# Kernel optimization log

Hardware: AMD Instinct MI355X
Metric: run time of the kernel (lower is better)

The kernel has to match this reference:

```python
import jax, jax.numpy as jnp
import numpy as np

NEG_INF = -1e9

def setup_inputs() -> dict:
    key = jax.random.key(0)
    k1, k2, k3, k4, k5 = jax.random.split(key, 5)
    N, F_IN, F_OUT, H = 8192, 128, 32, 4
    node_features = jax.random.normal(k1, (N, F_IN), dtype=jnp.float32)
    adj_matrix = jax.random.randint(k2, (N, N), 0, 2, dtype=jnp.int32)
    # stacked per-head params (original: one Linear W [F_IN,F_OUT] + attention vec a [2*F_OUT] per head)
    W = jax.random.normal(k3, (H, F_IN, F_OUT), dtype=jnp.float32) * (1.0 / np.sqrt(F_IN))
    a_src = jax.random.normal(k4, (H, F_OUT), dtype=jnp.float32) * 0.1
    a_dst = jax.random.normal(k5, (H, F_OUT), dtype=jnp.float32) * 0.1
    return {"node_features": node_features, "adj_matrix": adj_matrix,
            "W": W, "a_src": a_src, "a_dst": a_dst}

def reference(node_features, adj_matrix, W, a_src, a_dst):
    alpha = 0.2  # LeakyReLU negative slope
    # project: [H, N, F_OUT]
    h = jnp.einsum('nf,hfo->hno', node_features, W)
    # GAT scores e_ij = LeakyReLU(a_src . h_i + a_dst . h_j), shape [H, N, N]
    e_src = jnp.einsum('hno,ho->hn', h, a_src)  # [H, N]
    e_dst = jnp.einsum('hno,ho->hn', h, a_dst)  # [H, N]
    e = jax.nn.leaky_relu(e_src[:, :, None] + e_dst[:, None, :], negative_slope=alpha)
    mask = (adj_matrix > 0)[None, :, :]
    attn = jax.nn.softmax(jnp.where(mask, e, NEG_INF), axis=-1)  # [H, N, N]
    out = jnp.einsum('hij,hjo->hio', attn, h)  # [H, N, F_OUT]
    # concat heads along feature dim -> [N, H*F_OUT]
    H_, N_, O_ = out.shape
    return jnp.transpose(out, (1, 0, 2)).reshape(N_, H_ * O_)
```

## Files before the change

### kernel.cpp

```cpp
#include <hip/hip_runtime.h>
#include <hip/hip_bf16.h>

#define NTOT 8192
#define FIN 128
#define FOUT 32
#define NH 4
#define NSEG 4
#define LOG2E 1.4426950408889634f
#define BUFB 18432

typedef __attribute__((ext_vector_type(4))) float f32x4;
typedef __attribute__((ext_vector_type(4))) unsigned int u32x4;
typedef __attribute__((ext_vector_type(8))) __bf16 bf16x8;
typedef unsigned long long u64;
typedef unsigned int u32;

__device__ __forceinline__ unsigned short f2bf(float x) {
  __hip_bfloat16 h = __float2bfloat16(x);
  return *reinterpret_cast<unsigned short*>(&h);
}

__device__ __forceinline__ float fexp2(float y) {
  float p;
  asm("v_exp_f32 %0, %1" : "=v"(p) : "v"(y));
  return p;
}

__global__ __launch_bounds__(512, 2) void k0_pack(
    const int* __restrict__ adj, u64* __restrict__ bits64T) {
  int row = blockIdx.x * 8 + (threadIdx.x >> 6);
  int l = threadIdx.x & 63;
  const int* ap = adj + (size_t)row * NTOT + l;
  u64* bp = bits64T + row;
#pragma unroll 4
  for (int j64 = 0; j64 < NTOT / 64; ++j64) {
    int v = ap[j64 * 64];
    u64 mske = __ballot(v != 0);
    if (l == 0) bp[(size_t)j64 * NTOT] = mske;
  }
}

__global__ __launch_bounds__(256, 2) void k1_project(
    const float* __restrict__ X, const float* __restrict__ W,
    float* __restrict__ h, unsigned short* __restrict__ panel) {
  __shared__ float Xs[32 * 128];
  __shared__ float Ws[32 * 128];
  __shared__ unsigned short Hs[128 * 40];
  int t = threadIdx.x;
  int nb = blockIdx.x * 32;

  const f32x4* Xg = reinterpret_cast<const f32x4*>(X + (size_t)nb * FIN);
  f32x4* Xs4 = reinterpret_cast<f32x4*>(Xs);
#pragma unroll
  for (int r = 0; r < 4; ++r) Xs4[t + r * 256] = Xg[t + r * 256];

  int ng = t >> 5, oq = t & 31;
  int n0 = ng * 4, o0 = oq * 4;
  f32x4 acc[4];
#pragma unroll
  for (int nn = 0; nn < 4; ++nn) acc[nn] = (f32x4){0.f, 0.f, 0.f, 0.f};

  for (int kp = 0; kp < 4; ++kp) {
    __syncthreads();
#pragma unroll
    for (int r = 0; r < 4; ++r) {
      int q = t + r * 256;
      int flat = q * 4;
      int kk = flat >> 7;
      int c = flat & 127;
      int hdd = c >> 5;
      int oo = c & 31;
      *reinterpret_cast<f32x4*>(&Ws[kk * 128 + c]) =
          *reinterpret_cast<const f32x4*>(W + hdd * (FIN * FOUT) +
                                          (kp * 32 + kk) * FOUT + oo);
    }
    __syncthreads();
#pragma unroll 8
    for (int kk = 0; kk < 32; ++kk) {
      f32x4 wv = *reinterpret_cast<const f32x4*>(&Ws[kk * 128 + o0]);
#pragma unroll
      for (int nn = 0; nn < 4; ++nn)
        acc[nn] += Xs[(n0 + nn) * 128 + kp * 32 + kk] * wv;
    }
  }
#pragma unroll
  for (int nn = 0; nn < 4; ++nn) {
    *reinterpret_cast<f32x4*>(&h[(size_t)(nb + n0 + nn) * 128 + o0]) = acc[nn];
#pragma unroll
    for (int c = 0; c < 4; ++c)
      Hs[(o0 + c) * 40 + (n0 + nn)] = f2bf(acc[nn][c]);
  }
  __syncthreads();
  int jt = blockIdx.x;
#pragma unroll
  for (int it = 0; it < 2; ++it) {
    int item = t + it * 256;
    int p = item >> 6;
    int l = item & 63;
    int o = p * 16 + (l & 15);
    u32x4 v = *reinterpret_cast<const u32x4*>(&Hs[o * 40 + (l >> 4) * 8]);
    *reinterpret_cast<u32x4*>(panel + (size_t)(p * 256 + jt) * 512 + l * 8) = v;
  }
}

__global__ __launch_bounds__(256, 2) void k2_scores(
    const float* __restrict__ h, const float* __restrict__ a_src,
    const float* __restrict__ a_dst, float* __restrict__ Sl2,
    float* __restrict__ Dt) {
  int n = blockIdx.x * 256 + threadIdx.x;
  const f32x4* hv = reinterpret_cast<const f32x4*>(h + (size_t)n * 128);
  const f32x4* as4 = reinterpret_cast<const f32x4*>(a_src);
  const f32x4* ad4 = reinterpret_cast<const f32x4*>(a_dst);
#pragma unroll
  for (int hd = 0; hd < NH; ++hd) {
    f32x4 sa = {0.f, 0.f, 0.f, 0.f}, da = {0.f, 0.f, 0.f, 0.f};
#pragma unroll
    for (int q = 0; q < 8; ++q) {
      f32x4 x = hv[hd * 8 + q];
      sa += x * as4[hd * 8 + q];
      da += x * ad4[hd * 8 + q];
    }
    float s = (sa[0] + sa[1]) + (sa[2] + sa[3]);
    float d = (da[0] + da[1]) + (da[2] + da[3]);
    Sl2[hd * NTOT + n] = s * LOG2E;
    Dt[(n >> 6) * 256 + hd * 64 + (n & 63)] = d * LOG2E;
  }
}

__global__ __launch_bounds__(512)
__attribute__((amdgpu_waves_per_eu(4, 4))) void k3_attn(
    const u64* __restrict__ bits64T, const float* __restrict__ Sl2,
    const float* __restrict__ Dt, const unsigned short* __restrict__ panel,
    float* __restrict__ pacc, float* __restrict__ plsum) {
  const int N = NTOT;
  __shared__ char smem[2 * BUFB];
  int tid = threadIdx.x;
  int w = tid >> 6, l = tid & 63;
  int hd = w & 3, isub = w >> 2;
  int itile = blockIdx.x >> 2, seg = blockIdx.x & 3;
  int ibase = itile * 64 + isub * 32;
  int iblk = itile * 64;
  int m = l & 15, jc = (l >> 4) * 8;
  int i0 = ibase + m, i1 = i0 + 16;
  float sv0 = Sl2[hd * N + i0], sv1 = Sl2[hd * N + i1];
  int seg0 = seg * 32;

  const char* psrc =
      (const char*)panel + ((size_t)w * 256) * 1024 + (size_t)l * 16;
  const char* dsrc = (const char*)Dt + (size_t)l * 16;
  const u64* bsrc = bits64T + iblk + l;

  f32x4 z4 = {0.f, 0.f, 0.f, 0.f};
  f32x4 acc0[2] = {z4, z4}, acc1[2] = {z4, z4}, acc2[2] = {z4, z4};
  bf16x8 bones;
  {
    u32 pat = (m == 0) ? 0x3f803f80u : 0u;
    u32x4 tmp = {pat, pat, pat, pat};
    bones = *reinterpret_cast<bf16x8*>(&tmp);
  }

  u32x4 Pr0, Pr1, Dr;
  u64 Br;

#define LOADR(t_)                                              \
  {                                                            \
    int tc_ = (t_) > 31 ? 31 : (t_);                           \
    size_t jm_ = (size_t)(seg0 + tc_);                         \
    Pr0 = *(const u32x4*)(psrc + jm_ * 2048);                  \
    Pr1 = *(const u32x4*)(psrc + jm_ * 2048 + 1024);           \
    if (w == 0) Br = bsrc[jm_ * N];                            \
    if (w == 1) Dr = *(const u32x4*)(dsrc + jm_ * 1024);       \
  }

#define DSW(cb_)                                               \
  {                                                            \
    char* b_ = smem + (cb_)*BUFB;                              \
    *(u32x4*)(b_ + w * 2048 + l * 16) = Pr0;                   \
    *(u32x4*)(b_ + w * 2048 + 1024 + l * 16) = Pr1;            \
    if (w == 0) *(u64*)(b_ + 17408 + l * 8) = Br;              \
    if (w == 1) *(u32x4*)(b_ + 16384 + l * 16) = Dr;           \
  }

#define K3_AF(AF, BY, DA, DB, SV)                                        \
  {                                                                      \
    f32x4 xa_ = (DA) + (SV);                                             \
    f32x4 xb_ = (DB) + (SV);                                             \
    f32x4 ya_ = __builtin_elementwise_max(xa_, 0.2f * xa_);              \
    f32x4 yb_ = __builtin_elementwise_max(xb_, 0.2f * xb_);              \
    bf16x8 af_;                                                          \
    _Pragma("unroll") for (int e = 0; e < 4; ++e) af_[e] =               \
        (__bf16)fexp2(ya_[e]);                                           \
    _Pragma("unroll") for (int e = 0; e < 4; ++e) af_[e + 4] =           \
        (__bf16)fexp2(yb_[e]);                                           \
    u32x4 mk_;                                                           \
    _Pragma("unroll") for (int p = 0; p < 4; ++p) {                      \
      u32 lo_ = (u32)(((int)((BY) << (31 - 2 * p))) >> 31);              \
      u32 hi_ = (u32)(((int)((BY) << (30 - 2 * p))) >> 31);              \
      mk_[p] = __builtin_amdgcn_perm(hi_, lo_, 0x07060100u);             \
    }                                                                    \
    u32x4 av_ = *reinterpret_cast<u32x4*>(&af_) & mk_;                   \
    AF = *reinterpret_cast<bf16x8*>(&av_);                               \
  }

#define K3_RG(AF, B0, B1, RG)                                                \
  acc0[RG] =                                                                 \
      __builtin_amdgcn_mfma_f32_16x16x32_bf16(AF, (B0), acc0[RG], 0, 0, 0);  \
  acc1[RG] =                                                                 \
      __builtin_amdgcn_mfma_f32_16x16x32_bf16(AF, (B1), acc1[RG], 0, 0, 0);  \
  acc2[RG] =                                                                 \
      __builtin_amdgcn_mfma_f32_16x16x32_bf16(AF, bones, acc2[RG], 0, 0, 0);

#define COMPUTE(cb_)                                                     \
  {                                                                      \
    const char* b_ = smem + (cb_)*BUFB;                                  \
    u64 w0 = *(const u64*)(b_ + 17408 + (isub * 32 + m) * 8);            \
    u64 w1 = *(const u64*)(b_ + 17408 + (isub * 32 + 16 + m) * 8);       \
    const char* dp_ = b_ + 16384 + hd * 256 + jc * 4;                    \
    f32x4 d0 = *(const f32x4*)(dp_);                                     \
    f32x4 d1 = *(const f32x4*)(dp_ + 16);                                \
    f32x4 d2 = *(const f32x4*)(dp_ + 128);                               \
    f32x4 d3 = *(const f32x4*)(dp_ + 144);                               \
    const char* pp_ = b_ + (hd * 2) * 2048 + l * 16;                     \
    bf16x8 B0a = *(const bf16x8*)(pp_);                                  \
    bf16x8 B0b = *(const bf16x8*)(pp_ + 1024);                           \
    bf16x8 B1a = *(const bf16x8*)(pp_ + 2048);                           \
    bf16x8 B1b = *(const bf16x8*)(pp_ + 3072);                           \
    bf16x8 af_r;                                                         \
    u32 by_;                                                             \
    by_ = ((u32)w0 >> jc) & 0xFFu;                                       \
    K3_AF(af_r, by_, d0, d1, sv0) K3_RG(af_r, B0a, B1a, 0)               \
    by_ = ((u32)w1 >> jc) & 0xFFu;                                       \
    K3_AF(af_r, by_, d0, d1, sv1) K3_RG(af_r, B0a, B1a, 1)               \
    by_ = ((u32)(w0 >> 32) >> jc) & 0xFFu;                               \
    K3_AF(af_r, by_, d2, d3, sv0) K3_RG(af_r, B0b, B1b, 0)               \
    by_ = ((u32)(w1 >> 32) >> jc) & 0xFFu;                               \
    K3_AF(af_r, by_, d2, d3, sv1) K3_RG(af_r, B0b, B1b, 1)               \
  }

  LOADR(0);
  DSW(0);
  LOADR(1);
  __syncthreads();

#pragma unroll 1
  for (int t = 0; t < 32; ++t) {
    int cur = t & 1;
    COMPUTE(cur);
    DSW(cur ^ 1);
    LOADR(t + 2);
    __syncthreads();
  }
#undef LOADR
#undef DSW
#undef K3_AF
#undef K3_RG
#undef COMPUTE

#pragma unroll
  for (int rg = 0; rg < 2; ++rg) {
    int rb = ibase + rg * 16 + ((l >> 4) << 2);
    if (m == 0) {
#pragma unroll
      for (int r = 0; r < 4; ++r)
        plsum[(seg * NH + hd) * N + rb + r] = acc2[rg][r];
    }
#pragma unroll
    for (int r = 0; r < 4; ++r) {
      int row = rb + r;
      pacc[((size_t)seg * N + row) * 128 + hd * 32 + m] = acc0[rg][r];
      pacc[((size_t)seg * N + row) * 128 + hd * 32 + 16 + m] = acc1[rg][r];
    }
  }
}

__global__ __launch_bounds__(256, 2) void k4_combine(
    const float* __restrict__ pacc, const float* __restrict__ plsum,
    float* __restrict__ out) {
  int idx = blockIdx.x * 256 + threadIdx.x;
  int i = idx >> 7;
  int c = idx & 127;
  int hd = c >> 5;
  float a = 0.f, ls = 0.f;
#pragma unroll
  for (int s = 0; s < NSEG; ++s) {
    a += pacc[((size_t)s * NTOT + i) * 128 + c];
    ls += plsum[(s * NH + hd) * NTOT + i];
  }
  out[idx] = (ls > 0.f) ? a / ls : 0.f;
}

extern "C" void kernel_launch(void* const* d_in, const int* in_sizes, int n_in,
                              void* d_out, int out_size, void* d_ws,
                              size_t ws_size, hipStream_t stream) {
  const float* X = (const float*)d_in[0];
  const int* adj = (const int*)d_in[1];
  const float* W = (const float*)d_in[2];
  const float* a_src = (const float*)d_in[3];
  const float* a_dst = (const float*)d_in[4];
  float* out = (float*)d_out;

  char* ws = (char*)d_ws;
  float* h = (float*)(ws + 0x0);
  unsigned short* panel = (unsigned short*)(ws + 0x400000);
  float* Sl2 = (float*)(ws + 0x600000);
  float* Dt = (float*)(ws + 0x620000);
  u64* bits64T = (u64*)(ws + 0x640000);
  float* pacc = (float*)(ws + 0xE40000);
  float* plsum = (float*)(ws + 0x1E40000);

  k0_pack<<<dim3(1024), dim3(512), 0, stream>>>(adj, bits64T);
  k1_project<<<dim3(256), dim3(256), 0, stream>>>(X, W, h, panel);
  k2_scores<<<dim3(32), dim3(256), 0, stream>>>(h, a_src, a_dst, Sl2, Dt);
  k3_attn<<<dim3(128 * NSEG), dim3(512), 0, stream>>>(bits64T, Sl2, Dt, panel,
                                                      pacc, plsum);
  k4_combine<<<dim3(4096), dim3(256), 0, stream>>>(pacc, plsum, out);
}
```

Before: 178.3 us.

## Restructure attention kernel to per-wave async LDS DMA with no block barriers

The attention kernel now runs 4 waves per block, one per head, and each wave covers all 64 rows instead of 32, so the B operands from LDS are reused across four row groups. Tile data (panel, Dt, adjacency bits) goes straight from global memory into each wave's private double-buffered LDS region through global_load_lds DMA. Manual vmcnt waits replace __syncthreads, so no register staging or block-wide barrier is needed. In exchange, each wave holds more accumulators and issues redundant Dt and bitmask loads per head. Occupancy is pinned to 2 waves per EU, and correctness depends on the hand-counted vmcnt values.

```diff
diff --git a/kernel.cpp b/kernel.cpp
--- a/kernel.cpp
+++ b/kernel.cpp
@@ -7,7 +7,7 @@
 #define NH 4
 #define NSEG 4
 #define LOG2E 1.4426950408889634f
-#define BUFB 18432
+#define WBUF 4864
 
 typedef __attribute__((ext_vector_type(4))) float f32x4;
 typedef __attribute__((ext_vector_type(4))) unsigned int u32x4;
@@ -24,6 +24,17 @@
   float p;
   asm("v_exp_f32 %0, %1" : "=v"(p) : "v"(y));
   return p;
+}
+
+__device__ __forceinline__ void dma16(const void* g, void* l) {
+  __builtin_amdgcn_global_load_lds(
+      (const __attribute__((address_space(1))) void*)g,
+      (__attribute__((address_space(3))) void*)l, 16, 0, 0);
+}
+__device__ __forceinline__ void dma4(const void* g, void* l) {
+  __builtin_amdgcn_global_load_lds(
+      (const __attribute__((address_space(1))) void*)g,
+      (__attribute__((address_space(3))) void*)l, 4, 0, 0);
 }
 
 __global__ __launch_bounds__(512, 2) void k0_pack(
@@ -127,31 +138,35 @@
   }
 }
 
-__global__ __launch_bounds__(512)
-__attribute__((amdgpu_waves_per_eu(4, 4))) void k3_attn(
+__global__ __launch_bounds__(256)
+__attribute__((amdgpu_waves_per_eu(2, 2))) void k3_attn(
     const u64* __restrict__ bits64T, const float* __restrict__ Sl2,
     const float* __restrict__ Dt, const unsigned short* __restrict__ panel,
     float* __restrict__ pacc, float* __restrict__ plsum) {
   const int N = NTOT;
-  __shared__ char smem[2 * BUFB];
+  __shared__ char smem[4 * 2 * WBUF];
   int tid = threadIdx.x;
-  int w = tid >> 6, l = tid & 63;
-  int hd = w & 3, isub = w >> 2;
+  int hd = tid >> 6, l = tid & 63;
   int itile = blockIdx.x >> 2, seg = blockIdx.x & 3;
-  int ibase = itile * 64 + isub * 32;
-  int iblk = itile * 64;
+  int ibase = itile * 64;
   int m = l & 15, jc = (l >> 4) * 8;
-  int i0 = ibase + m, i1 = i0 + 16;
-  float sv0 = Sl2[hd * N + i0], sv1 = Sl2[hd * N + i1];
+  char* wbase = smem + hd * (2 * WBUF);
+
+  float sv0 = Sl2[hd * N + ibase + m];
+  float sv1 = Sl2[hd * N + ibase + 16 + m];
+  float sv2 = Sl2[hd * N + ibase + 32 + m];
+  float sv3 = Sl2[hd * N + ibase + 48 + m];
+  asm volatile("" : "+v"(sv0), "+v"(sv1), "+v"(sv2), "+v"(sv3));
   int seg0 = seg * 32;
 
-  const char* psrc =
-      (const char*)panel + ((size_t)w * 256) * 1024 + (size_t)l * 16;
-  const char* dsrc = (const char*)Dt + (size_t)l * 16;
-  const u64* bsrc = bits64T + iblk + l;
+  const char* pg0 = (const char*)panel + (size_t)(hd * 2) * 262144;
+  const char* pg1 = pg0 + 262144;
+  const char* dg = (const char*)Dt;
+  const char* bg = (const char*)bits64T;
 
   f32x4 z4 = {0.f, 0.f, 0.f, 0.f};
-  f32x4 acc0[2] = {z4, z4}, acc1[2] = {z4, z4}, acc2[2] = {z4, z4};
+  f32x4 acc0[4] = {z4, z4, z4, z4}, acc1[4] = {z4, z4, z4, z4},
+        acc2[4] = {z4, z4, z4, z4};
   bf16x8 bones;
   {
     u32 pat = (m == 0) ? 0x3f803f80u : 0u;
@@ -159,26 +174,44 @@
     bones = *reinterpret_cast<bf16x8*>(&tmp);
   }
 
-  u32x4 Pr0, Pr1, Dr;
-  u64 Br;
-
-#define LOADR(t_)                                              \
-  {                                                            \
-    int tc_ = (t_) > 31 ? 31 : (t_);                           \
-    size_t jm_ = (size_t)(seg0 + tc_);                         \
-    Pr0 = *(const u32x4*)(psrc + jm_ * 2048);                  \
-    Pr1 = *(const u32x4*)(psrc + jm_ * 2048 + 1024);           \
-    if (w == 0) Br = bsrc[jm_ * N];                            \
-    if (w == 1) Dr = *(const u32x4*)(dsrc + jm_ * 1024);       \
-  }
-
-#define DSW(cb_)                                               \
-  {                                                            \
-    char* b_ = smem + (cb_)*BUFB;                              \
-    *(u32x4*)(b_ + w * 2048 + l * 16) = Pr0;                   \
-    *(u32x4*)(b_ + w * 2048 + 1024 + l * 16) = Pr1;            \
-    if (w == 0) *(u64*)(b_ + 17408 + l * 8) = Br;              \
-    if (w == 1) *(u32x4*)(b_ + 16384 + l * 16) = Dr;           \
+#define STAGE(t_)                                                      \
+  {                                                                    \
+    int tc_ = (t_) > 31 ? 31 : (t_);                                   \
+    size_t jm_ = (size_t)(seg0 + tc_);                                 \
+    char* lb_ = wbase + ((t_)&1) * WBUF;                               \
+    const char* g0_ = pg0 + jm_ * 2048 + (size_t)l * 16;               \
+    const char* g1_ = pg1 + jm_ * 2048 + (size_t)l * 16;               \
+    dma16(g0_, lb_);                                                   \
+    dma16(g0_ + 1024, lb_ + 1024);                                     \
+    dma16(g1_, lb_ + 2048);                                            \
+    dma16(g1_ + 1024, lb_ + 3072);                                     \
+    dma4(dg + jm_ * 1024 + hd * 256 + (size_t)l * 4, lb_ + 4096);      \
+    const char* gb_ = bg + (jm_ * N + ibase) * 8;                      \
+    dma4(gb_ + (size_t)l * 4, lb_ + 4352);                             \
+    dma4(gb_ + 256 + (size_t)l * 4, lb_ + 4608);                       \
+  }
+
+  u64 wr0, wr1, wr2, wr3;
+  f32x4 d0, d1, d2, d3;
+  bf16x8 B0a, B0b, B1a, B1b;
+
+#define LDSREAD(cb_)                                                   \
+  {                                                                    \
+    const char* b_ = wbase + (cb_)*WBUF;                               \
+    wr0 = *(const u64*)(b_ + 4352 + m * 8);                            \
+    wr1 = *(const u64*)(b_ + 4352 + 128 + m * 8);                      \
+    wr2 = *(const u64*)(b_ + 4352 + 256 + m * 8);                      \
+    wr3 = *(const u64*)(b_ + 4352 + 384 + m * 8);                      \
+    const char* dp_ = b_ + 4096 + jc * 4;                              \
+    d0 = *(const f32x4*)(dp_);                                         \
+    d1 = *(const f32x4*)(dp_ + 16);                                    \
+    d2 = *(const f32x4*)(dp_ + 128);                                   \
+    d3 = *(const f32x4*)(dp_ + 144);                                   \
+    const char* pp_ = b_ + (size_t)l * 16;                             \
+    B0a = *(const bf16x8*)(pp_);                                       \
+    B0b = *(const bf16x8*)(pp_ + 1024);                                \
+    B1a = *(const bf16x8*)(pp_ + 2048);                                \
+    B1b = *(const bf16x8*)(pp_ + 3072);                                \
   }
 
 #define K3_AF(AF, BY, DA, DB, SV)                                        \
@@ -202,62 +235,52 @@
     AF = *reinterpret_cast<bf16x8*>(&av_);                               \
   }
 
-#define K3_RG(AF, B0, B1, RG)                                                \
-  acc0[RG] =                                                                 \
-      __builtin_amdgcn_mfma_f32_16x16x32_bf16(AF, (B0), acc0[RG], 0, 0, 0);  \
-  acc1[RG] =                                                                 \
-      __builtin_amdgcn_mfma_f32_16x16x32_bf16(AF, (B1), acc1[RG], 0, 0, 0);  \
-  acc2[RG] =                                                                 \
-      __builtin_amdgcn_mfma_f32_16x16x32_bf16(AF, bones, acc2[RG], 0, 0, 0);
-
-#define COMPUTE(cb_)                                                     \
-  {                                                                      \
-    const char* b_ = smem + (cb_)*BUFB;                                  \
-    u64 w0 = *(const u64*)(b_ + 17408 + (isub * 32 + m) * 8);            \
-    u64 w1 = *(const u64*)(b_ + 17408 + (isub * 32 + 16 + m) * 8);       \
-    const char* dp_ = b_ + 16384 + hd * 256 + jc * 4;                    \
-    f32x4 d0 = *(const f32x4*)(dp_);                                     \
-    f32x4 d1 = *(const f32x4*)(dp_ + 16);                                \
-    f32x4 d2 = *(const f32x4*)(dp_ + 128);                               \
-    f32x4 d3 = *(const f32x4*)(dp_ + 144);                               \
-    const char* pp_ = b_ + (hd * 2) * 2048 + l * 16;                     \
-    bf16x8 B0a = *(const bf16x8*)(pp_);                                  \
-    bf16x8 B0b = *(const bf16x8*)(pp_ + 1024);                           \
-    bf16x8 B1a = *(const bf16x8*)(pp_ + 2048);                           \
-    bf16x8 B1b = *(const bf16x8*)(pp_ + 3072);                           \
-    bf16x8 af_r;                                                         \
-    u32 by_;                                                             \
-    by_ = ((u32)w0 >> jc) & 0xFFu;                                       \
-    K3_AF(af_r, by_, d0, d1, sv0) K3_RG(af_r, B0a, B1a, 0)               \
-    by_ = ((u32)w1 >> jc) & 0xFFu;                                       \
-    K3_AF(af_r, by_, d0, d1, sv1) K3_RG(af_r, B0a, B1a, 1)               \
-    by_ = ((u32)(w0 >> 32) >> jc) & 0xFFu;                               \
-    K3_AF(af_r, by_, d2, d3, sv0) K3_RG(af_r, B0b, B1b, 0)               \
-    by_ = ((u32)(w1 >> 32) >> jc) & 0xFFu;                               \
-    K3_AF(af_r, by_, d2, d3, sv1) K3_RG(af_r, B0b, B1b, 1)               \
-  }
-
-  LOADR(0);
-  DSW(0);
-  LOADR(1);
-  __syncthreads();
+#define MATH_RG(RG, WR, SV)                                                  \
+  {                                                                          \
+    bf16x8 af_r;                                                             \
+    u32 by_ = ((u32)(WR) >> jc) & 0xFFu;                                     \
+    K3_AF(af_r, by_, d0, d1, SV)                                             \
+    acc0[RG] =                                                               \
+        __builtin_amdgcn_mfma_f32_16x16x32_bf16(af_r, B0a, acc0[RG], 0, 0, 0); \
+    acc1[RG] =                                                               \
+        __builtin_amdgcn_mfma_f32_16x16x32_bf16(af_r, B1a, acc1[RG], 0, 0, 0); \
+    acc2[RG] = __builtin_amdgcn_mfma_f32_16x16x32_bf16(af_r, bones,          \
+                                                       acc2[RG], 0, 0, 0);   \
+    by_ = ((u32)((WR) >> 32) >> jc) & 0xFFu;                                 \
+    K3_AF(af_r, by_, d2, d3, SV)                                             \
+    acc0[RG] =                                                               \
+        __builtin_amdgcn_mfma_f32_16x16x32_bf16(af_r, B0b, acc0[RG], 0, 0, 0); \
+    acc1[RG] =                                                               \
+        __builtin_amdgcn_mfma_f32_16x16x32_bf16(af_r, B1b, acc1[RG], 0, 0, 0); \
+    acc2[RG] = __builtin_amdgcn_mfma_f32_16x16x32_bf16(af_r, bones,          \
+                                                       acc2[RG], 0, 0, 0);   \
+  }
+
+  STAGE(0)
+  STAGE(1)
 
 #pragma unroll 1
   for (int t = 0; t < 32; ++t) {
     int cur = t & 1;
-    COMPUTE(cur);
-    DSW(cur ^ 1);
-    LOADR(t + 2);
-    __syncthreads();
-  }
-#undef LOADR
-#undef DSW
+    asm volatile("s_waitcnt vmcnt(7)" ::: "memory");
+    LDSREAD(cur)
+    asm volatile("s_waitcnt lgkmcnt(0)" ::: "memory");
+    __builtin_amdgcn_sched_barrier(0);
+    STAGE(t + 2)
+    MATH_RG(0, wr0, sv0)
+    MATH_RG(1, wr1, sv1)
+    MATH_RG(2, wr2, sv2)
+    MATH_RG(3, wr3, sv3)
+  }
+#undef STAGE
+#undef LDSREAD
 #undef K3_AF
-#undef K3_RG
-#undef COMPUTE
-
-#pragma unroll
-  for (int rg = 0; rg < 2; ++rg) {
+#undef MATH_RG
+
+  asm volatile("s_waitcnt vmcnt(0)" ::: "memory");
+
+#pragma unroll
+  for (int rg = 0; rg < 4; ++rg) {
     int rb = ibase + rg * 16 + ((l >> 4) << 2);
     if (m == 0) {
 #pragma unroll
@@ -311,7 +334,7 @@
   k0_pack<<<dim3(1024), dim3(512), 0, stream>>>(adj, bits64T);
   k1_project<<<dim3(256), dim3(256), 0, stream>>>(X, W, h, panel);
   k2_scores<<<dim3(32), dim3(256), 0, stream>>>(h, a_src, a_dst, Sl2, Dt);
-  k3_attn<<<dim3(128 * NSEG), dim3(512), 0, stream>>>(bits64T, Sl2, Dt, panel,
+  k3_attn<<<dim3(128 * NSEG), dim3(256), 0, stream>>>(bits64T, Sl2, Dt, panel,
                                                       pacc, plsum);
   k4_combine<<<dim3(4096), dim3(256), 0, stream>>>(pacc, plsum, out);
 }
```

Result: no change. 178.2 us (-0.1%).

## Fuse adjacency bit-packing into attention kernel and drop LDS staging

Applied to the files above, without the earlier changes.

Removes the separate bit-packing kernel and has the attention kernel read the int32 adjacency rows directly, using a select to -1e9 before exp for masking. Each wave now owns 16 rows across all four heads, with the panel and Dt loaded straight from global memory instead of being staged through shared memory with barriers. Adjacency loads are double-buffered in registers. The aim is to avoid the extra pass that writes and re-reads the packed mask, plus the block synchronisation. The cost is that the attention kernel now streams the full 256MB int32 adjacency itself, and the panel and Dt are re-read per wave from cache.

```diff
diff --git a/kernel.cpp b/kernel.cpp
--- a/kernel.cpp
+++ b/kernel.cpp
@@ -6,10 +6,11 @@
 #define FOUT 32
 #define NH 4
 #define NSEG 4
+#define SEGJ (NTOT / NSEG)
 #define LOG2E 1.4426950408889634f
-#define BUFB 18432
 
 typedef __attribute__((ext_vector_type(4))) float f32x4;
+typedef __attribute__((ext_vector_type(4))) int i32x4;
 typedef __attribute__((ext_vector_type(4))) unsigned int u32x4;
 typedef __attribute__((ext_vector_type(8))) __bf16 bf16x8;
 typedef unsigned long long u64;
@@ -24,20 +25,6 @@
   float p;
   asm("v_exp_f32 %0, %1" : "=v"(p) : "v"(y));
   return p;
-}
-
-__global__ __launch_bounds__(512, 2) void k0_pack(
-    const int* __restrict__ adj, u64* __restrict__ bits64T) {
-  int row = blockIdx.x * 8 + (threadIdx.x >> 6);
-  int l = threadIdx.x & 63;
-  const int* ap = adj + (size_t)row * NTOT + l;
-  u64* bp = bits64T + row;
-#pragma unroll 4
-  for (int j64 = 0; j64 < NTOT / 64; ++j64) {
-    int v = ap[j64 * 64];
-    u64 mske = __ballot(v != 0);
-    if (l == 0) bp[(size_t)j64 * NTOT] = mske;
-  }
 }
 
 __global__ __launch_bounds__(256, 2) void k1_project(
@@ -127,31 +114,29 @@
   }
 }
 
-__global__ __launch_bounds__(512)
-__attribute__((amdgpu_waves_per_eu(4, 4))) void k3_attn(
-    const u64* __restrict__ bits64T, const float* __restrict__ Sl2,
+__global__ __launch_bounds__(256)
+__attribute__((amdgpu_waves_per_eu(2, 2))) void k3_attn(
+    const int* __restrict__ adj, const float* __restrict__ Sl2,
     const float* __restrict__ Dt, const unsigned short* __restrict__ panel,
     float* __restrict__ pacc, float* __restrict__ plsum) {
   const int N = NTOT;
-  __shared__ char smem[2 * BUFB];
   int tid = threadIdx.x;
   int w = tid >> 6, l = tid & 63;
-  int hd = w & 3, isub = w >> 2;
   int itile = blockIdx.x >> 2, seg = blockIdx.x & 3;
-  int ibase = itile * 64 + isub * 32;
-  int iblk = itile * 64;
-  int m = l & 15, jc = (l >> 4) * 8;
-  int i0 = ibase + m, i1 = i0 + 16;
-  float sv0 = Sl2[hd * N + i0], sv1 = Sl2[hd * N + i1];
+  int ibase = itile * 64;
+  int m = l & 15, g = l >> 4, jc = g * 8;
+  int row = ibase + w * 16 + m;
   int seg0 = seg * 32;
 
-  const char* psrc =
-      (const char*)panel + ((size_t)w * 256) * 1024 + (size_t)l * 16;
-  const char* dsrc = (const char*)Dt + (size_t)l * 16;
-  const u64* bsrc = bits64T + iblk + l;
+  float svv[4];
+#pragma unroll
+  for (int hd = 0; hd < 4; ++hd) svv[hd] = Sl2[hd * N + row];
+
+  const int* adjr = adj + (size_t)row * N + seg * SEGJ + jc;
 
   f32x4 z4 = {0.f, 0.f, 0.f, 0.f};
-  f32x4 acc0[2] = {z4, z4}, acc1[2] = {z4, z4}, acc2[2] = {z4, z4};
+  f32x4 c0[4] = {z4, z4, z4, z4}, c1[4] = {z4, z4, z4, z4},
+        cs[4] = {z4, z4, z4, z4};
   bf16x8 bones;
   {
     u32 pat = (m == 0) ? 0x3f803f80u : 0u;
@@ -159,116 +144,91 @@
     bones = *reinterpret_cast<bf16x8*>(&tmp);
   }
 
-  u32x4 Pr0, Pr1, Dr;
-  u64 Br;
-
-#define LOADR(t_)                                              \
+  i32x4 Aa0, Aa1, Aa2, Aa3, Ba0, Ba1, Ba2, Ba3;
+
+#define AISS(P, t_)                                            \
   {                                                            \
     int tc_ = (t_) > 31 ? 31 : (t_);                           \
-    size_t jm_ = (size_t)(seg0 + tc_);                         \
-    Pr0 = *(const u32x4*)(psrc + jm_ * 2048);                  \
-    Pr1 = *(const u32x4*)(psrc + jm_ * 2048 + 1024);           \
-    if (w == 0) Br = bsrc[jm_ * N];                            \
-    if (w == 1) Dr = *(const u32x4*)(dsrc + jm_ * 1024);       \
-  }
-
-#define DSW(cb_)                                               \
-  {                                                            \
-    char* b_ = smem + (cb_)*BUFB;                              \
-    *(u32x4*)(b_ + w * 2048 + l * 16) = Pr0;                   \
-    *(u32x4*)(b_ + w * 2048 + 1024 + l * 16) = Pr1;            \
-    if (w == 0) *(u64*)(b_ + 17408 + l * 8) = Br;              \
-    if (w == 1) *(u32x4*)(b_ + 16384 + l * 16) = Dr;           \
-  }
-
-#define K3_AF(AF, BY, DA, DB, SV)                                        \
+    const int* a_ = adjr + tc_ * 64;                           \
+    P##a0 = *reinterpret_cast<const i32x4*>(a_);               \
+    P##a1 = *reinterpret_cast<const i32x4*>(a_ + 4);           \
+    P##a2 = *reinterpret_cast<const i32x4*>(a_ + 32);          \
+    P##a3 = *reinterpret_cast<const i32x4*>(a_ + 36);          \
+  }                                                            \
+  __builtin_amdgcn_sched_barrier(0);
+
+#define AFSEL(AF, AV0, AV1, DA, DB, SV)                                  \
   {                                                                      \
     f32x4 xa_ = (DA) + (SV);                                             \
     f32x4 xb_ = (DB) + (SV);                                             \
     f32x4 ya_ = __builtin_elementwise_max(xa_, 0.2f * xa_);              \
     f32x4 yb_ = __builtin_elementwise_max(xb_, 0.2f * xb_);              \
-    bf16x8 af_;                                                          \
-    _Pragma("unroll") for (int e = 0; e < 4; ++e) af_[e] =               \
-        (__bf16)fexp2(ya_[e]);                                           \
-    _Pragma("unroll") for (int e = 0; e < 4; ++e) af_[e + 4] =           \
-        (__bf16)fexp2(yb_[e]);                                           \
-    u32x4 mk_;                                                           \
-    _Pragma("unroll") for (int p = 0; p < 4; ++p) {                      \
-      u32 lo_ = (u32)(((int)((BY) << (31 - 2 * p))) >> 31);              \
-      u32 hi_ = (u32)(((int)((BY) << (30 - 2 * p))) >> 31);              \
-      mk_[p] = __builtin_amdgcn_perm(hi_, lo_, 0x07060100u);             \
+    _Pragma("unroll") for (int e = 0; e < 4; ++e) {                      \
+      float y_ = ((AV0)[e] != 0) ? ya_[e] : -1e9f;                       \
+      AF[e] = (__bf16)fexp2(y_);                                         \
     }                                                                    \
-    u32x4 av_ = *reinterpret_cast<u32x4*>(&af_) & mk_;                   \
-    AF = *reinterpret_cast<bf16x8*>(&av_);                               \
-  }
-
-#define K3_RG(AF, B0, B1, RG)                                                \
-  acc0[RG] =                                                                 \
-      __builtin_amdgcn_mfma_f32_16x16x32_bf16(AF, (B0), acc0[RG], 0, 0, 0);  \
-  acc1[RG] =                                                                 \
-      __builtin_amdgcn_mfma_f32_16x16x32_bf16(AF, (B1), acc1[RG], 0, 0, 0);  \
-  acc2[RG] =                                                                 \
-      __builtin_amdgcn_mfma_f32_16x16x32_bf16(AF, bones, acc2[RG], 0, 0, 0);
-
-#define COMPUTE(cb_)                                                     \
-  {                                                                      \
-    const char* b_ = smem + (cb_)*BUFB;                                  \
-    u64 w0 = *(const u64*)(b_ + 17408 + (isub * 32 + m) * 8);            \
-    u64 w1 = *(const u64*)(b_ + 17408 + (isub * 32 + 16 + m) * 8);       \
-    const char* dp_ = b_ + 16384 + hd * 256 + jc * 4;                    \
-    f32x4 d0 = *(const f32x4*)(dp_);                                     \
-    f32x4 d1 = *(const f32x4*)(dp_ + 16);                                \
-    f32x4 d2 = *(const f32x4*)(dp_ + 128);                               \
-    f32x4 d3 = *(const f32x4*)(dp_ + 144);                               \
-    const char* pp_ = b_ + (hd * 2) * 2048 + l * 16;                     \
-    bf16x8 B0a = *(const bf16x8*)(pp_);                                  \
-    bf16x8 B0b = *(const bf16x8*)(pp_ + 1024);                           \
-    bf16x8 B1a = *(const bf16x8*)(pp_ + 2048);                           \
-    bf16x8 B1b = *(const bf16x8*)(pp_ + 3072);                           \
-    bf16x8 af_r;                                                         \
-    u32 by_;                                                             \
-    by_ = ((u32)w0 >> jc) & 0xFFu;                                       \
-    K3_AF(af_r, by_, d0, d1, sv0) K3_RG(af_r, B0a, B1a, 0)               \
-    by_ = ((u32)w1 >> jc) & 0xFFu;                                       \
-    K3_AF(af_r, by_, d0, d1, sv1) K3_RG(af_r, B0a, B1a, 1)               \
-    by_ = ((u32)(w0 >> 32) >> jc) & 0xFFu;                               \
-    K3_AF(af_r, by_, d2, d3, sv0) K3_RG(af_r, B0b, B1b, 0)               \
-    by_ = ((u32)(w1 >> 32) >> jc) & 0xFFu;                               \
-    K3_AF(af_r, by_, d2, d3, sv1) K3_RG(af_r, B0b, B1b, 1)               \
-  }
-
-  LOADR(0);
-  DSW(0);
-  LOADR(1);
-  __syncthreads();
-
+    _Pragma("unroll") for (int e = 0; e < 4; ++e) {                      \
+      float y_ = ((AV1)[e] != 0) ? yb_[e] : -1e9f;                       \
+      AF[e + 4] = (__bf16)fexp2(y_);                                     \
+    }                                                                    \
+  }
+
+#define MFM(AF, B, ACC) \
+  ACC = __builtin_amdgcn_mfma_f32_16x16x32_bf16(AF, B, ACC, 0, 0, 0);
+
+#define MATHM(P, t_)                                                       \
+  {                                                                       \
+    int jm_ = seg0 + (t_);                                                \
+    const float* db_ = Dt + (size_t)jm_ * 256;                            \
+    const unsigned short* pb_ =                                           \
+        panel + (size_t)(seg * 64 + (t_)*2) * 512 + l * 8;                \
+    _Pragma("unroll") for (int hd = 0; hd < 4; ++hd) {                    \
+      f32x4 d0 = *(const f32x4*)(db_ + hd * 64 + jc);                     \
+      f32x4 d1 = *(const f32x4*)(db_ + hd * 64 + jc + 4);                 \
+      f32x4 d2 = *(const f32x4*)(db_ + hd * 64 + 32 + jc);                \
+      f32x4 d3 = *(const f32x4*)(db_ + hd * 64 + 32 + jc + 4);            \
+      const unsigned short* p0_ = pb_ + (size_t)(hd * 2) * 131072;        \
+      const unsigned short* p1_ = pb_ + (size_t)(hd * 2 + 1) * 131072;    \
+      bf16x8 B0a = *(const bf16x8*)(p0_);                                 \
+      bf16x8 B1a = *(const bf16x8*)(p1_);                                 \
+      bf16x8 B0b = *(const bf16x8*)(p0_ + 512);                           \
+      bf16x8 B1b = *(const bf16x8*)(p1_ + 512);                           \
+      float sv_ = svv[hd];                                                \
+      bf16x8 af_;                                                         \
+      AFSEL(af_, P##a0, P##a1, d0, d1, sv_)                               \
+      MFM(af_, B0a, c0[hd]) MFM(af_, B1a, c1[hd]) MFM(af_, bones, cs[hd]) \
+      AFSEL(af_, P##a2, P##a3, d2, d3, sv_)                               \
+      MFM(af_, B0b, c0[hd]) MFM(af_, B1b, c1[hd]) MFM(af_, bones, cs[hd]) \
+    }                                                                     \
+  }
+
+  AISS(A, 0)
+  AISS(B, 1)
 #pragma unroll 1
-  for (int t = 0; t < 32; ++t) {
-    int cur = t & 1;
-    COMPUTE(cur);
-    DSW(cur ^ 1);
-    LOADR(t + 2);
-    __syncthreads();
-  }
-#undef LOADR
-#undef DSW
-#undef K3_AF
-#undef K3_RG
-#undef COMPUTE
-
-#pragma unroll
-  for (int rg = 0; rg < 2; ++rg) {
-    int rb = ibase + rg * 16 + ((l >> 4) << 2);
+  for (int tt = 0; tt < 16; ++tt) {
+    MATHM(A, 2 * tt)
+    AISS(A, 2 * tt + 2)
+    MATHM(B, 2 * tt + 1)
+    AISS(B, 2 * tt + 3)
+  }
+#undef AISS
+#undef AFSEL
+#undef MFM
+#undef MATHM
+
+#pragma unroll
+  for (int hd = 0; hd < 4; ++hd) {
+    int rb = ibase + w * 16 + g * 4;
     if (m == 0) {
 #pragma unroll
       for (int r = 0; r < 4; ++r)
-        plsum[(seg * NH + hd) * N + rb + r] = acc2[rg][r];
+        plsum[(seg * NH + hd) * N + rb + r] = cs[hd][r];
     }
 #pragma unroll
     for (int r = 0; r < 4; ++r) {
-      int row = rb + r;
-      pacc[((size_t)seg * N + row) * 128 + hd * 32 + m] = acc0[rg][r];
-      pacc[((size_t)seg * N + row) * 128 + hd * 32 + 16 + m] = acc1[rg][r];
+      int rowr = rb + r;
+      pacc[((size_t)seg * N + rowr) * 128 + hd * 32 + m] = c0[hd][r];
+      pacc[((size_t)seg * N + rowr) * 128 + hd * 32 + 16 + m] = c1[hd][r];
     }
   }
 }
@@ -304,14 +264,12 @@
   unsigned short* panel = (unsigned short*)(ws + 0x400000);
   float* Sl2 = (float*)(ws + 0x600000);
   float* Dt = (float*)(ws + 0x620000);
-  u64* bits64T = (u64*)(ws + 0x640000);
   float* pacc = (float*)(ws + 0xE40000);
   float* plsum = (float*)(ws + 0x1E40000);
 
-  k0_pack<<<dim3(1024), dim3(512), 0, stream>>>(adj, bits64T);
   k1_project<<<dim3(256), dim3(256), 0, stream>>>(X, W, h, panel);
   k2_scores<<<dim3(32), dim3(256), 0, stream>>>(h, a_src, a_dst, Sl2, Dt);
-  k3_attn<<<dim3(128 * NSEG), dim3(512), 0, stream>>>(bits64T, Sl2, Dt, panel,
+  k3_attn<<<dim3(128 * NSEG), dim3(256), 0, stream>>>(adj, Sl2, Dt, panel,
                                                       pacc, plsum);
   k4_combine<<<dim3(4096), dim3(256), 0, stream>>>(pacc, plsum, out);
 }
```

Measured after the change: 146.5 us. 1.22x faster.
